# Optimization experiments

Hardware: AMD Instinct MI355X
Metric: run time of the kernel (lower is better)

Reference implementation:

```python
import jax, jax.numpy as jnp
import numpy as np

N = 100000
E = 1600000
D = 128
H = 64
C = 10
G = 1024  # number of graphs in the batch


def setup_inputs() -> dict:
    key = jax.random.key(0)
    ks = jax.random.split(key, 12)
    x = jax.random.normal(ks[0], (N, D), dtype=jnp.float32)
    edge_index = jax.random.randint(ks[1], (2, E), 0, N, dtype=jnp.int64)
    batch = jnp.sort(jax.random.randint(ks[2], (N,), 0, G, dtype=jnp.int64))
    def glorot(k, fan_in, fan_out):
        s = jnp.sqrt(6.0 / (fan_in + fan_out))
        return jax.random.uniform(k, (fan_in, fan_out), jnp.float32, -s, s)
    W1 = glorot(ks[3], D, H); b1 = jnp.zeros((H,), jnp.float32)
    W2 = glorot(ks[4], H, H); b2 = jnp.zeros((H,), jnp.float32)
    W3 = glorot(ks[5], H, H); b3 = jnp.zeros((H,), jnp.float32)
    Wl = glorot(ks[6], H, C); bl = jnp.zeros((C,), jnp.float32)
    return {"x": x, "edge_index": edge_index, "batch": batch,
            "W1": W1, "b1": b1, "W2": W2, "b2": b2,
            "W3": W3, "b3": b3, "Wl": Wl, "bl": bl}


def gcn_conv(x, row, col, dinv, W, b):
    # PyG GCNConv: x' = D^-1/2 (A + I) D^-1/2 (x W) + b
    xw = x @ W                                   # (N, H)
    norm = dinv[row] * dinv[col]                 # (E+N,)
    msg = xw[row] * norm[:, None]                # gather + scale
    out = jax.ops.segment_sum(msg, col, num_segments=N)
    return out + b


def reference(x, edge_index, batch, W1, b1, W2, b2, W3, b3, Wl, bl):
    # add self loops once; normalization coefficients shared by all layers
    loop = jnp.arange(N, dtype=edge_index.dtype)
    row = jnp.concatenate([edge_index[0], loop])
    col = jnp.concatenate([edge_index[1], loop])
    deg = jax.ops.segment_sum(jnp.ones_like(col, dtype=x.dtype), col, num_segments=N)
    dinv = jnp.where(deg > 0, jax.lax.rsqrt(deg), 0.0)

    h = gcn_conv(x, row, col, dinv, W1, b1)
    h = gcn_conv(h, row, col, dinv, W2, b2)
    h = gcn_conv(h, row, col, dinv, W3, b3)

    # global mean pool over graphs
    sums = jax.ops.segment_sum(h, batch, num_segments=G)          # (G, H)
    cnts = jax.ops.segment_sum(jnp.ones((N,), h.dtype), batch, num_segments=G)
    pooled = sums / jnp.maximum(cnts, 1.0)[:, None]

    # dropout(p=0.5) is identity in eval mode
    return pooled @ Wl + bl                                        # (G, C)
```

## Files before the change

kernel.cpp:

```cpp
#include <hip/hip_runtime.h>

#define NN 100000
#define EE 1600000
#define DI 128
#define HH 64
#define CO 10
#define PAD 12
#define GG 1024
#define BSH 7
#define BNODES (1 << BSH)
#define NB ((NN + BNODES - 1) / BNODES)
#define TILE 16384
#define NT ((EE + TILE - 1) / TILE)
#define SN (NB * NT)
#define SCB 1024
#define NSB ((SN + SCB - 1) / SCB)
#define LPN 8

__global__ void k_small_mats(const float* __restrict__ W1, const float* __restrict__ W2,
                             const float* __restrict__ W3, const float* __restrict__ Wl,
                             const float* __restrict__ b1, const float* __restrict__ b2,
                             const float* __restrict__ b3,
                             float* __restrict__ Wf, float* __restrict__ cvec) {
    __shared__ float M3l[HH * CO];
    __shared__ float M23l[HH * CO];
    int t = threadIdx.x;
    for (int i = t; i < HH * CO; i += blockDim.x) {
        int r = i / CO, c = i % CO;
        float s = 0.f;
        for (int k = 0; k < HH; ++k) s += W3[r * HH + k] * Wl[k * CO + c];
        M3l[i] = s;
    }
    __syncthreads();
    for (int i = t; i < HH * CO; i += blockDim.x) {
        int r = i / CO, c = i % CO;
        float s = 0.f;
        for (int k = 0; k < HH; ++k) s += W2[r * HH + k] * M3l[k * CO + c];
        M23l[i] = s;
    }
    __syncthreads();
    for (int i = t; i < DI * CO; i += blockDim.x) {
        int r = i / CO, c = i % CO;
        float s = 0.f;
        for (int k = 0; k < HH; ++k) s += W1[r * HH + k] * M23l[k * CO + c];
        Wf[i] = s;
    }
    if (t < CO) {
        float s1 = 0.f, s2 = 0.f, s3 = 0.f;
        for (int k = 0; k < HH; ++k) {
            s1 += b1[k] * M23l[k * CO + t];
            s2 += b2[k] * M3l[k * CO + t];
            s3 += b3[k] * Wl[k * CO + t];
        }
        cvec[t] = s1; cvec[CO + t] = s2; cvec[2 * CO + t] = s3;
    }
}

__global__ __launch_bounds__(256) void k_pcount(const int* __restrict__ col, int* __restrict__ cnt) {
    __shared__ int h[NB];
    for (int i = threadIdx.x; i < NB; i += 256) h[i] = 0;
    __syncthreads();
    int base = blockIdx.x * TILE;
    int end = min(base + TILE, EE);
    for (int e = base + threadIdx.x; e < end; e += 256)
        atomicAdd(&h[__builtin_nontemporal_load(&col[e]) >> BSH], 1);
    __syncthreads();
    for (int i = threadIdx.x; i < NB; i += 256)
        cnt[i * NT + blockIdx.x] = h[i];
}

__global__ __launch_bounds__(SCB) void k_scanA(int* __restrict__ a, int* __restrict__ bsum) {
    __shared__ int s[SCB];
    int t = threadIdx.x, idx = blockIdx.x * SCB + t;
    int v = (idx < SN) ? a[idx] : 0;
    s[t] = v;
    __syncthreads();
    for (int off = 1; off < SCB; off <<= 1) {
        int u = (t >= off) ? s[t - off] : 0;
        __syncthreads();
        s[t] += u;
        __syncthreads();
    }
    if (idx < SN) a[idx] = s[t] - v;
    if (t == SCB - 1) bsum[blockIdx.x] = s[t];
}
__global__ __launch_bounds__(128) void k_scanB(int* __restrict__ bsum) {
    __shared__ int s[128];
    int t = threadIdx.x;
    int v = (t < NSB) ? bsum[t] : 0;
    s[t] = v;
    __syncthreads();
    for (int off = 1; off < 128; off <<= 1) {
        int u = (t >= off) ? s[t - off] : 0;
        __syncthreads();
        s[t] += u;
        __syncthreads();
    }
    if (t < NSB) bsum[t] = s[t] - v;
}
__global__ __launch_bounds__(SCB) void k_scanC(int* __restrict__ a, const int* __restrict__ bsum) {
    int idx = blockIdx.x * SCB + threadIdx.x;
    if (idx < SN) a[idx] += bsum[blockIdx.x];
}

__global__ __launch_bounds__(256) void k_pscatter(const int* __restrict__ row, const int* __restrict__ col,
                                                  const int* __restrict__ S, unsigned* __restrict__ ebuf) {
    __shared__ int ofs[NB];
    for (int i = threadIdx.x; i < NB; i += 256) ofs[i] = S[i * NT + blockIdx.x];
    __syncthreads();
    int base = blockIdx.x * TILE;
    int end = min(base + TILE, EE);
    for (int e = base + threadIdx.x; e < end; e += 256) {
        int c = __builtin_nontemporal_load(&col[e]);
        int r = __builtin_nontemporal_load(&row[e]);
        int pos = atomicAdd(&ofs[c >> BSH], 1);
        ebuf[pos] = ((unsigned)r << BSH) | (unsigned)(c & (BNODES - 1));
    }
}

__global__ __launch_bounds__(256) void k_bsort(const unsigned* __restrict__ ebuf, const int* __restrict__ S,
                                               int* __restrict__ srcIdx, int* __restrict__ rowptr_end,
                                               float* __restrict__ dinv) {
    __shared__ int cnt[BNODES];
    __shared__ int s[BNODES];
    __shared__ int ofs[BNODES];
    int t = threadIdx.x;
    int b = blockIdx.x;
    if (t < BNODES) cnt[t] = 0;
    __syncthreads();
    int beg = S[b * NT];
    int end = (b + 1 < NB) ? S[(b + 1) * NT] : EE;
    for (int e = beg + t; e < end; e += 256)
        atomicAdd(&cnt[__builtin_nontemporal_load(&ebuf[e]) & (BNODES - 1)], 1);
    __syncthreads();
    int v = 0;
    if (t < BNODES) { v = cnt[t]; s[t] = v; }
    __syncthreads();
    for (int off = 1; off < BNODES; off <<= 1) {
        int u = 0;
        if (t < BNODES && t >= off) u = s[t - off];
        __syncthreads();
        if (t < BNODES) s[t] += u;
        __syncthreads();
    }
    if (t < BNODES) {
        int n = (b << BSH) + t;
        if (n < NN) {
            dinv[n] = rsqrtf((float)(v + 1));
            rowptr_end[n] = beg + s[t];
        }
        ofs[t] = beg + s[t] - v;
    }
    __syncthreads();
    for (int e = beg + t; e < end; e += 256) {
        unsigned p = __builtin_nontemporal_load(&ebuf[e]);
        int pos = atomicAdd(&ofs[p & (BNODES - 1)], 1);
        srcIdx[pos] = (int)(p >> BSH);
    }
}

__global__ void k_gstart(const int* __restrict__ batch, int* __restrict__ gstart) {
    int g = blockIdx.x * blockDim.x + threadIdx.x;
    if (g > GG) return;
    int lo = 0, hi = NN;
    while (lo < hi) { int mid = (lo + hi) >> 1; if (batch[mid] < g) lo = mid + 1; else hi = mid; }
    gstart[g] = lo;
}

__global__ __launch_bounds__(256) void k_xw(const float* __restrict__ x, const float* __restrict__ Wf,
                                            const float* __restrict__ dinv,
                                            float* __restrict__ as_) {
    __shared__ float sWf[DI * CO];
    for (int i = threadIdx.x; i < DI * CO; i += blockDim.x) sWf[i] = Wf[i];
    __syncthreads();
    int n = blockIdx.x * blockDim.x + threadIdx.x;
    if (n >= NN) return;
    float acc[CO];
#pragma unroll
    for (int c = 0; c < CO; ++c) acc[c] = 0.f;
    const float4* xr = (const float4*)(x + (size_t)n * DI);
#pragma unroll 4
    for (int d4 = 0; d4 < DI / 4; ++d4) {
        float4 v = xr[d4];
        int d = d4 * 4;
#pragma unroll
        for (int c = 0; c < CO; ++c)
            acc[c] += v.x * sWf[(d + 0) * CO + c] + v.y * sWf[(d + 1) * CO + c]
                    + v.z * sWf[(d + 2) * CO + c] + v.w * sWf[(d + 3) * CO + c];
    }
    float di = dinv[n];
    float* o = as_ + (size_t)n * PAD;
    ((float4*)o)[0] = make_float4(acc[0] * di, acc[1] * di, acc[2] * di, acc[3] * di);
    ((float4*)o)[1] = make_float4(acc[4] * di, acc[5] * di, acc[6] * di, acc[7] * di);
    ((float2*)(o + 8))[0] = make_float2(acc[8] * di, acc[9] * di);
}

template <int FINAL>
__global__ __launch_bounds__(256) void k_gather(const int* __restrict__ rowptr_end,
                                                const int* __restrict__ srcIdx,
                                                const float* __restrict__ src,
                                                const float* __restrict__ dinv,
                                                const float* __restrict__ cvec, int coff,
                                                float* __restrict__ dst) {
    int gid = blockIdx.x * blockDim.x + threadIdx.x;
    int n = gid / LPN;
    int l = threadIdx.x & (LPN - 1);
    if (n >= NN) return;
    int beg = (n == 0) ? 0 : rowptr_end[n - 1];
    int end = rowptr_end[n];
    float acc[CO];
#pragma unroll
    for (int c = 0; c < CO; ++c) acc[c] = 0.f;
    for (int e = beg + l; e < end; e += LPN) {
        int s = __builtin_nontemporal_load(&srcIdx[e]);
        const float* sp = src + (size_t)s * PAD;
        float4 a = ((const float4*)sp)[0];
        float4 b = ((const float4*)sp)[1];
        float2 c2 = ((const float2*)(sp + 8))[0];
        acc[0] += a.x; acc[1] += a.y; acc[2] += a.z; acc[3] += a.w;
        acc[4] += b.x; acc[5] += b.y; acc[6] += b.z; acc[7] += b.w;
        acc[8] += c2.x; acc[9] += c2.y;
    }
#pragma unroll
    for (int m = 1; m < LPN; m <<= 1) {
#pragma unroll
        for (int c = 0; c < CO; ++c) acc[c] += __shfl_xor(acc[c], m, 64);
    }
    if (l == 0) {
        float di = dinv[n];
        const float* selfp = src + (size_t)n * PAD;
        float o[CO];
#pragma unroll
        for (int c = 0; c < CO; ++c) {
            float y = di * (acc[c] + selfp[c]) + cvec[coff + c];
            o[c] = FINAL ? y : y * di;
        }
        float* dp = dst + (size_t)n * PAD;
        ((float4*)dp)[0] = make_float4(o[0], o[1], o[2], o[3]);
        ((float4*)dp)[1] = make_float4(o[4], o[5], o[6], o[7]);
        ((float2*)(dp + 8))[0] = make_float2(o[8], o[9]);
    }
}

__global__ __launch_bounds__(64) void k_pool(const float* __restrict__ h,
                                             const int* __restrict__ gstart,
                                             const float* __restrict__ bl,
                                             float* __restrict__ out) {
    int g = blockIdx.x;
    int beg = gstart[g], end = gstart[g + 1];
    int l = threadIdx.x;
    float acc[CO];
#pragma unroll
    for (int c = 0; c < CO; ++c) acc[c] = 0.f;
    for (int n = beg + l; n < end; n += 64) {
        const float* sp = h + (size_t)n * PAD;
        float4 a = ((const float4*)sp)[0];
        float4 b = ((const float4*)sp)[1];
        float2 c2 = ((const float2*)(sp + 8))[0];
        acc[0] += a.x; acc[1] += a.y; acc[2] += a.z; acc[3] += a.w;
        acc[4] += b.x; acc[5] += b.y; acc[6] += b.z; acc[7] += b.w;
        acc[8] += c2.x; acc[9] += c2.y;
    }
#pragma unroll
    for (int m = 1; m < 64; m <<= 1) {
#pragma unroll
        for (int c = 0; c < CO; ++c) acc[c] += __shfl_xor(acc[c], m, 64);
    }
    if (l == 0) {
        float cf = fmaxf((float)(end - beg), 1.f);
#pragma unroll
        for (int c = 0; c < CO; ++c) out[(size_t)g * CO + c] = acc[c] / cf + bl[c];
    }
}

extern "C" void kernel_launch(void* const* d_in, const int* in_sizes, int n_in,
                              void* d_out, int out_size, void* d_ws, size_t ws_size,
                              hipStream_t stream) {
    const float* x    = (const float*)d_in[0];
    const int*   ei   = (const int*)d_in[1];
    const int*   batch= (const int*)d_in[2];
    const float* W1   = (const float*)d_in[3];
    const float* b1   = (const float*)d_in[4];
    const float* W2   = (const float*)d_in[5];
    const float* b2   = (const float*)d_in[6];
    const float* W3   = (const float*)d_in[7];
    const float* b3   = (const float*)d_in[8];
    const float* Wl   = (const float*)d_in[9];
    const float* bl   = (const float*)d_in[10];
    float* out = (float*)d_out;

    const int* row = ei;
    const int* col = ei + EE;

    float* ws = (float*)d_ws;
    size_t off = 0;
    auto alloc = [&](size_t elems) { size_t cur = off; off += (elems + 63) & ~(size_t)63; return cur; };
    float*    Wf      = ws + alloc(DI * CO);
    float*    cvec    = ws + alloc(3 * CO);
    float*    dinv    = ws + alloc(NN);
    int*      S       = (int*)(ws + alloc(SN));
    int*      bsum    = (int*)(ws + alloc(128));
    unsigned* ebuf    = (unsigned*)(ws + alloc(EE));
    int*      srcIdx  = (int*)(ws + alloc(EE));
    int*      rowptr  = (int*)(ws + alloc(NN));
    float*    as_     = ws + alloc((size_t)NN * PAD);
    float*    bbuf    = ws + alloc((size_t)NN * PAD);
    int*      gstart  = (int*)(ws + alloc(GG + 1));
    (void)ws_size; (void)in_sizes; (void)n_in; (void)out_size;

    const int BT = 256;
    int gN = (NN + BT - 1) / BT;
    int gNL = ((NN * LPN) + BT - 1) / BT;

    hipLaunchKernelGGL(k_small_mats, dim3(1), dim3(256), 0, stream, W1, W2, W3, Wl, b1, b2, b3, Wf, cvec);
    hipLaunchKernelGGL(k_pcount,   dim3(NT),  dim3(256), 0, stream, col, S);
    hipLaunchKernelGGL(k_scanA,    dim3(NSB), dim3(SCB), 0, stream, S, bsum);
    hipLaunchKernelGGL(k_scanB,    dim3(1),   dim3(128), 0, stream, bsum);
    hipLaunchKernelGGL(k_scanC,    dim3(NSB), dim3(SCB), 0, stream, S, bsum);
    hipLaunchKernelGGL(k_pscatter, dim3(NT),  dim3(256), 0, stream, row, col, S, ebuf);
    hipLaunchKernelGGL(k_bsort,    dim3(NB),  dim3(256), 0, stream, ebuf, S, srcIdx, rowptr, dinv);
    hipLaunchKernelGGL(k_gstart,   dim3((GG + 1 + BT - 1) / BT), dim3(BT), 0, stream, batch, gstart);
    hipLaunchKernelGGL(k_xw,       dim3(gN),  dim3(BT), 0, stream, x, Wf, dinv, as_);

    hipLaunchKernelGGL((k_gather<0>), dim3(gNL), dim3(BT), 0, stream, rowptr, srcIdx, as_,  dinv, cvec, 0,      bbuf);
    hipLaunchKernelGGL((k_gather<0>), dim3(gNL), dim3(BT), 0, stream, rowptr, srcIdx, bbuf, dinv, cvec, CO,     as_);
    hipLaunchKernelGGL((k_gather<1>), dim3(gNL), dim3(BT), 0, stream, rowptr, srcIdx, as_,  dinv, cvec, 2 * CO, bbuf);

    hipLaunchKernelGGL(k_pool, dim3(GG), dim3(64), 0, stream, bbuf, gstart, bl, out);
}
```

Before: 299.5 us.

## Merge front-end kernels, split xw output columns across lanes, use 4 lanes per node

Combines the small-matrix fold, the per-tile column histogram and the graph-start binary search into one heterogeneous launch, dropping two kernel launches. The xw projection now has each thread handle two nodes and five of the ten output columns, so every loaded weight is reused across two rows. The gather kernels go from 8 to 4 lanes per node, so more nodes run per wave but each lane walks more edges serially. The fused front kernel makes one block do the serial matrix work while the other blocks do the histogram, and the xw change relies on NN being even.

```diff
diff --git a/kernel.cpp b/kernel.cpp
--- a/kernel.cpp
+++ b/kernel.cpp
@@ -5,7 +5,7 @@
 #define DI 128
 #define HH 64
 #define CO 10
-#define PAD 12
+#define PADF 12
 #define GG 1024
 #define BSH 7
 #define BNODES (1 << BSH)
@@ -15,58 +15,67 @@
 #define SN (NB * NT)
 #define SCB 1024
 #define NSB ((SN + SCB - 1) / SCB)
-#define LPN 8
-
-__global__ void k_small_mats(const float* __restrict__ W1, const float* __restrict__ W2,
-                             const float* __restrict__ W3, const float* __restrict__ Wl,
-                             const float* __restrict__ b1, const float* __restrict__ b2,
-                             const float* __restrict__ b3,
-                             float* __restrict__ Wf, float* __restrict__ cvec) {
-    __shared__ float M3l[HH * CO];
-    __shared__ float M23l[HH * CO];
-    int t = threadIdx.x;
-    for (int i = t; i < HH * CO; i += blockDim.x) {
-        int r = i / CO, c = i % CO;
-        float s = 0.f;
-        for (int k = 0; k < HH; ++k) s += W3[r * HH + k] * Wl[k * CO + c];
-        M3l[i] = s;
-    }
-    __syncthreads();
-    for (int i = t; i < HH * CO; i += blockDim.x) {
-        int r = i / CO, c = i % CO;
-        float s = 0.f;
-        for (int k = 0; k < HH; ++k) s += W2[r * HH + k] * M3l[k * CO + c];
-        M23l[i] = s;
-    }
-    __syncthreads();
-    for (int i = t; i < DI * CO; i += blockDim.x) {
-        int r = i / CO, c = i % CO;
-        float s = 0.f;
-        for (int k = 0; k < HH; ++k) s += W1[r * HH + k] * M23l[k * CO + c];
-        Wf[i] = s;
-    }
-    if (t < CO) {
-        float s1 = 0.f, s2 = 0.f, s3 = 0.f;
-        for (int k = 0; k < HH; ++k) {
-            s1 += b1[k] * M23l[k * CO + t];
-            s2 += b2[k] * M3l[k * CO + t];
-            s3 += b3[k] * Wl[k * CO + t];
-        }
-        cvec[t] = s1; cvec[CO + t] = s2; cvec[2 * CO + t] = s3;
-    }
-}
-
-__global__ __launch_bounds__(256) void k_pcount(const int* __restrict__ col, int* __restrict__ cnt) {
-    __shared__ int h[NB];
-    for (int i = threadIdx.x; i < NB; i += 256) h[i] = 0;
-    __syncthreads();
-    int base = blockIdx.x * TILE;
-    int end = min(base + TILE, EE);
-    for (int e = base + threadIdx.x; e < end; e += 256)
-        atomicAdd(&h[__builtin_nontemporal_load(&col[e]) >> BSH], 1);
-    __syncthreads();
-    for (int i = threadIdx.x; i < NB; i += 256)
-        cnt[i * NT + blockIdx.x] = h[i];
+#define LPN 4
+
+__global__ __launch_bounds__(256) void k_front(const int* __restrict__ col,
+                                               const float* __restrict__ W1, const float* __restrict__ W2,
+                                               const float* __restrict__ W3, const float* __restrict__ Wl,
+                                               const float* __restrict__ b1, const float* __restrict__ b2,
+                                               const float* __restrict__ b3,
+                                               const int* __restrict__ batch,
+                                               int* __restrict__ cnt, float* __restrict__ Wf,
+                                               float* __restrict__ cvec, int* __restrict__ gstart) {
+    __shared__ float smem[1280];
+    int bid = blockIdx.x, t = threadIdx.x;
+    if (bid < NT) {
+        int* h = (int*)smem;
+        for (int i = t; i < NB; i += 256) h[i] = 0;
+        __syncthreads();
+        int base = bid * TILE, end = min(base + TILE, EE);
+        for (int e = base + t; e < end; e += 256)
+            atomicAdd(&h[__builtin_nontemporal_load(&col[e]) >> BSH], 1);
+        __syncthreads();
+        for (int i = t; i < NB; i += 256) cnt[i * NT + bid] = h[i];
+    } else if (bid == NT) {
+        float* M3l = smem;
+        float* M23l = smem + 640;
+        for (int i = t; i < HH * CO; i += 256) {
+            int r = i / CO, c = i % CO;
+            float s = 0.f;
+            for (int k = 0; k < HH; ++k) s += W3[r * HH + k] * Wl[k * CO + c];
+            M3l[i] = s;
+        }
+        __syncthreads();
+        for (int i = t; i < HH * CO; i += 256) {
+            int r = i / CO, c = i % CO;
+            float s = 0.f;
+            for (int k = 0; k < HH; ++k) s += W2[r * HH + k] * M3l[k * CO + c];
+            M23l[i] = s;
+        }
+        __syncthreads();
+        for (int i = t; i < DI * CO; i += 256) {
+            int r = i / CO, c = i % CO;
+            float s = 0.f;
+            for (int k = 0; k < HH; ++k) s += W1[r * HH + k] * M23l[k * CO + c];
+            Wf[i] = s;
+        }
+        if (t < CO) {
+            float s1 = 0.f, s2 = 0.f, s3 = 0.f;
+            for (int k = 0; k < HH; ++k) {
+                s1 += b1[k] * M23l[k * CO + t];
+                s2 += b2[k] * M3l[k * CO + t];
+                s3 += b3[k] * Wl[k * CO + t];
+            }
+            cvec[t] = s1; cvec[CO + t] = s2; cvec[2 * CO + t] = s3;
+        }
+    } else {
+        int g = (bid - NT - 1) * 256 + t;
+        if (g <= GG) {
+            int lo = 0, hi = NN;
+            while (lo < hi) { int mid = (lo + hi) >> 1; if (batch[mid] < g) lo = mid + 1; else hi = mid; }
+            gstart[g] = lo;
+        }
+    }
 }
 
 __global__ __launch_bounds__(SCB) void k_scanA(int* __restrict__ a, int* __restrict__ bsum) {
@@ -159,40 +168,38 @@
     }
 }
 
-__global__ void k_gstart(const int* __restrict__ batch, int* __restrict__ gstart) {
-    int g = blockIdx.x * blockDim.x + threadIdx.x;
-    if (g > GG) return;
-    int lo = 0, hi = NN;
-    while (lo < hi) { int mid = (lo + hi) >> 1; if (batch[mid] < g) lo = mid + 1; else hi = mid; }
-    gstart[g] = lo;
-}
-
 __global__ __launch_bounds__(256) void k_xw(const float* __restrict__ x, const float* __restrict__ Wf,
                                             const float* __restrict__ dinv,
                                             float* __restrict__ as_) {
     __shared__ float sWf[DI * CO];
     for (int i = threadIdx.x; i < DI * CO; i += blockDim.x) sWf[i] = Wf[i];
     __syncthreads();
-    int n = blockIdx.x * blockDim.x + threadIdx.x;
-    if (n >= NN) return;
-    float acc[CO];
-#pragma unroll
-    for (int c = 0; c < CO; ++c) acc[c] = 0.f;
-    const float4* xr = (const float4*)(x + (size_t)n * DI);
+    int gid = blockIdx.x * 256 + threadIdx.x;
+    if (gid >= NN) return;
+    int p = gid >> 1, c0 = (gid & 1) * 5;
+    int n0 = 2 * p, n1 = n0 + 1;
+    float a0[5] = {0, 0, 0, 0, 0}, a1[5] = {0, 0, 0, 0, 0};
+    const float4* x0 = (const float4*)(x + (size_t)n0 * DI);
+    const float4* x1 = (const float4*)(x + (size_t)n1 * DI);
 #pragma unroll 4
     for (int d4 = 0; d4 < DI / 4; ++d4) {
-        float4 v = xr[d4];
-        int d = d4 * 4;
-#pragma unroll
-        for (int c = 0; c < CO; ++c)
-            acc[c] += v.x * sWf[(d + 0) * CO + c] + v.y * sWf[(d + 1) * CO + c]
-                    + v.z * sWf[(d + 2) * CO + c] + v.w * sWf[(d + 3) * CO + c];
-    }
-    float di = dinv[n];
-    float* o = as_ + (size_t)n * PAD;
-    ((float4*)o)[0] = make_float4(acc[0] * di, acc[1] * di, acc[2] * di, acc[3] * di);
-    ((float4*)o)[1] = make_float4(acc[4] * di, acc[5] * di, acc[6] * di, acc[7] * di);
-    ((float2*)(o + 8))[0] = make_float2(acc[8] * di, acc[9] * di);
+        float4 u = x0[d4], v = x1[d4];
+        const float* w = &sWf[d4 * 4 * CO + c0];
+#pragma unroll
+        for (int c = 0; c < 5; ++c) {
+            float w0 = w[c], w1 = w[CO + c], w2 = w[2 * CO + c], w3 = w[3 * CO + c];
+            a0[c] += u.x * w0 + u.y * w1 + u.z * w2 + u.w * w3;
+            a1[c] += v.x * w0 + v.y * w1 + v.z * w2 + v.w * w3;
+        }
+    }
+    float d0 = dinv[n0], d1 = dinv[n1];
+    float* r0 = as_ + (size_t)n0 * PADF + c0;
+    float* r1 = as_ + (size_t)n1 * PADF + c0;
+#pragma unroll
+    for (int c = 0; c < 5; ++c) {
+        r0[c] = a0[c] * d0;
+        r1[c] = a1[c] * d1;
+    }
 }
 
 template <int FINAL>
@@ -202,8 +209,8 @@
                                                 const float* __restrict__ dinv,
                                                 const float* __restrict__ cvec, int coff,
                                                 float* __restrict__ dst) {
-    int gid = blockIdx.x * blockDim.x + threadIdx.x;
-    int n = gid / LPN;
+    int gid = blockIdx.x * 256 + threadIdx.x;
+    int n = gid >> 2;
     int l = threadIdx.x & (LPN - 1);
     if (n >= NN) return;
     int beg = (n == 0) ? 0 : rowptr_end[n - 1];
@@ -213,7 +220,7 @@
     for (int c = 0; c < CO; ++c) acc[c] = 0.f;
     for (int e = beg + l; e < end; e += LPN) {
         int s = __builtin_nontemporal_load(&srcIdx[e]);
-        const float* sp = src + (size_t)s * PAD;
+        const float* sp = src + (size_t)s * PADF;
         float4 a = ((const float4*)sp)[0];
         float4 b = ((const float4*)sp)[1];
         float2 c2 = ((const float2*)(sp + 8))[0];
@@ -228,14 +235,14 @@
     }
     if (l == 0) {
         float di = dinv[n];
-        const float* selfp = src + (size_t)n * PAD;
+        const float* selfp = src + (size_t)n * PADF;
         float o[CO];
 #pragma unroll
         for (int c = 0; c < CO; ++c) {
             float y = di * (acc[c] + selfp[c]) + cvec[coff + c];
             o[c] = FINAL ? y : y * di;
         }
-        float* dp = dst + (size_t)n * PAD;
+        float* dp = dst + (size_t)n * PADF;
         ((float4*)dp)[0] = make_float4(o[0], o[1], o[2], o[3]);
         ((float4*)dp)[1] = make_float4(o[4], o[5], o[6], o[7]);
         ((float2*)(dp + 8))[0] = make_float2(o[8], o[9]);
@@ -253,7 +260,7 @@
 #pragma unroll
     for (int c = 0; c < CO; ++c) acc[c] = 0.f;
     for (int n = beg + l; n < end; n += 64) {
-        const float* sp = h + (size_t)n * PAD;
+        const float* sp = h + (size_t)n * PADF;
         float4 a = ((const float4*)sp)[0];
         float4 b = ((const float4*)sp)[1];
         float2 c2 = ((const float2*)(sp + 8))[0];
@@ -303,23 +310,23 @@
     unsigned* ebuf    = (unsigned*)(ws + alloc(EE));
     int*      srcIdx  = (int*)(ws + alloc(EE));
     int*      rowptr  = (int*)(ws + alloc(NN));
-    float*    as_     = ws + alloc((size_t)NN * PAD);
-    float*    bbuf    = ws + alloc((size_t)NN * PAD);
+    float*    as_     = ws + alloc((size_t)NN * PADF);
+    float*    bbuf    = ws + alloc((size_t)NN * PADF);
     int*      gstart  = (int*)(ws + alloc(GG + 1));
     (void)ws_size; (void)in_sizes; (void)n_in; (void)out_size;
 
     const int BT = 256;
     int gN = (NN + BT - 1) / BT;
     int gNL = ((NN * LPN) + BT - 1) / BT;
-
-    hipLaunchKernelGGL(k_small_mats, dim3(1), dim3(256), 0, stream, W1, W2, W3, Wl, b1, b2, b3, Wf, cvec);
-    hipLaunchKernelGGL(k_pcount,   dim3(NT),  dim3(256), 0, stream, col, S);
+    int gFront = NT + 1 + (GG + 1 + BT - 1) / BT;
+
+    hipLaunchKernelGGL(k_front,    dim3(gFront), dim3(256), 0, stream,
+                       col, W1, W2, W3, Wl, b1, b2, b3, batch, S, Wf, cvec, gstart);
     hipLaunchKernelGGL(k_scanA,    dim3(NSB), dim3(SCB), 0, stream, S, bsum);
     hipLaunchKernelGGL(k_scanB,    dim3(1),   dim3(128), 0, stream, bsum);
     hipLaunchKernelGGL(k_scanC,    dim3(NSB), dim3(SCB), 0, stream, S, bsum);
     hipLaunchKernelGGL(k_pscatter, dim3(NT),  dim3(256), 0, stream, row, col, S, ebuf);
     hipLaunchKernelGGL(k_bsort,    dim3(NB),  dim3(256), 0, stream, ebuf, S, srcIdx, rowptr, dinv);
-    hipLaunchKernelGGL(k_gstart,   dim3((GG + 1 + BT - 1) / BT), dim3(BT), 0, stream, batch, gstart);
     hipLaunchKernelGGL(k_xw,       dim3(gN),  dim3(BT), 0, stream, x, Wf, dinv, as_);
 
     hipLaunchKernelGGL((k_gather<0>), dim3(gNL), dim3(BT), 0, stream, rowptr, srcIdx, as_,  dinv, cvec, 0,      bbuf);
```

Result: faster. 283.7 us (-5.3%).
